# Optimization experiments

Hardware: AMD Instinct MI355X
Metric: run time of the kernel (lower is better)

Reference implementation:

```python
import jax, jax.numpy as jnp
import numpy as np

RADIUS = 0.4
NSHELLS = 3
GSCALE = 0.69314718056 * NSHELLS ** 2  # ln(2)*num_shells^2, as in TFN.__init__
KNN = 32          # patch_size
UNITS = 64        # per-type intertwiner width
STRIDE = 4        # source->target pooling ratio (num_points[i]/num_points[i+1])


def real_sh(d):
    """Real spherical harmonics up to l=3 on unit vectors d[...,3] -> [...,16]."""
    x, y, z = d[..., 0], d[..., 1], d[..., 2]
    x2, y2, z2 = x * x, y * y, z * z
    comps = [
        0.282095 * jnp.ones_like(x),                 # l=0
        0.488603 * y, 0.488603 * z, 0.488603 * x,    # l=1 (y,z,x)
        1.092548 * x * y,                            # l=2
        1.092548 * y * z,
        0.315392 * (3.0 * z2 - 1.0),
        1.092548 * x * z,
        0.546274 * (x2 - y2),
        0.590044 * y * (3.0 * x2 - y2),              # l=3
        2.890611 * x * y * z,
        0.457046 * y * (5.0 * z2 - 1.0),
        0.373176 * z * (5.0 * z2 - 3.0),
        0.457046 * x * (5.0 * z2 - 1.0),
        1.445306 * z * (x2 - y2),
        0.590044 * x * (x2 - 3.0 * y2),
    ]
    return jnp.stack(comps, axis=-1)


def setup_inputs() -> dict:
    key = jax.random.key(0)
    ks = jax.random.split(key, 16)
    B, N, C = 32, 2048, 64
    SC = NSHELLS * C  # channels after shell expansion
    FEAT = 4 * UNITS  # invariant feature dim (types 0..3)
    NUM_CLASSES = 40
    inp = {
        "points": jax.random.normal(ks[0], (B, N, 3), jnp.float32),
        "feats": 0.1 * jax.random.normal(ks[1], (B, N, C), jnp.float32),
        "W0": jax.random.normal(ks[2], (SC, UNITS), jnp.float32) / np.sqrt(SC),
        "b0": jnp.zeros((UNITS,), jnp.float32),
        "W1": jax.random.normal(ks[3], (SC, UNITS), jnp.float32) / np.sqrt(SC),
        "W2": jax.random.normal(ks[4], (SC, UNITS), jnp.float32) / np.sqrt(SC),
        "W3": jax.random.normal(ks[5], (SC, UNITS), jnp.float32) / np.sqrt(SC),
        "Wfc1": jax.random.normal(ks[6], (FEAT, 512), jnp.float32) / np.sqrt(FEAT),
        "bfc1": jnp.zeros((512,), jnp.float32),
        "Wfc2": jax.random.normal(ks[7], (512, 256), jnp.float32) / np.sqrt(512),
        "bfc2": jnp.zeros((256,), jnp.float32),
        "Wsm": jax.random.normal(ks[8], (256, NUM_CLASSES), jnp.float32) / np.sqrt(256),
        "bsm": jnp.zeros((NUM_CLASSES,), jnp.float32),
    }
    return inp


def reference(points, feats, W0, b0, W1, W2, W3, Wfc1, bfc1, Wfc2, bfc2, Wsm, bsm):
    # --- pooling: strided subsample (kd_pooling analogue) ---
    target = points[:, ::STRIDE]                       # [B,M,3]
    # --- ball-query style grouping: knn gather ---
    d2 = jnp.sum((target[:, :, None, :] - points[:, None, :, :]) ** 2, axis=-1)  # [B,M,N]
    _, idx = jax.lax.top_k(-d2, KNN)                   # [B,M,K]
    gat = jax.vmap(lambda a, i: a[i])
    p = gat(points, idx)                               # [B,M,K,3]
    f = gat(feats, idx)                                # [B,M,K,C]
    rel = p - target[:, :, None, :]
    dist = jnp.sqrt(jnp.maximum(jnp.sum(rel * rel, axis=-1), 1e-12))  # [B,M,K]
    dirs = rel / dist[..., None]
    # --- spherical-harmonic Gaussian shell kernels ---
    Y = real_sh(dirs)                                  # [B,M,K,16]
    centers = jnp.linspace(0.0, 1.0, NSHELLS)
    dn = dist / RADIUS
    w = jnp.exp(-GSCALE * (dn[..., None] - centers) ** 2)
    w = w * (dn <= 1.0)[..., None]                     # bounded kernel
    w = w / (jnp.sum(w, axis=2, keepdims=True) + 1e-8)  # normalize over patch
    kern = w[..., :, None] * Y[..., None, :]           # [B,M,K,S,16]
    # --- point conv: contract over patch dim ---
    z = jnp.einsum('bmksp,bmkc->bmpsc', kern, f)       # [B,M,16,S,C]
    B_, M_ = z.shape[:2]
    z = z.reshape(B_, M_, 16, -1)                      # [B,M,16,S*C]
    # --- per-type Dense intertwiners (bias only on type-0) + invariant norms ---
    slabs = [(0, 1, W0, b0), (1, 4, W1, None), (4, 9, W2, None), (9, 16, W3, None)]
    outs = []
    for s, e, W, b in slabs:
        o = z[:, :, s:e, :] @ W
        if b is not None:
            o = o + b
        outs.append(jnp.sqrt(jnp.maximum(jnp.sum(o * o, axis=2), 1e-8)))  # [B,M,U]
    h = jnp.concatenate(outs, axis=-1)                 # [B,M,4U]
    h = jnp.max(h, axis=1)                             # global max pool
    # --- MLP head ---
    h = jax.nn.relu(h @ Wfc1 + bfc1)
    h = jax.nn.relu(h @ Wfc2 + bfc2)
    return jax.nn.softmax(h @ Wsm + bsm, axis=-1)
```

## Files before the change

kernel.cpp:

```cpp
#include <hip/hip_runtime.h>
#include <hip/hip_bf16.h>
#include <math.h>

#define B_ 32
#define N_ 2048
#define C_ 64
#define M_ 512
#define KNN_ 32
#define RADIUS_ 0.4f
#define RCUT2 0.16016f
#define GSCALE_ 6.2383246250f
#define TT 4
#define NWAVE 8
#define SEGCAP 40
#define NBLK 4096

typedef __attribute__((ext_vector_type(8))) short bf16x8;
typedef __attribute__((ext_vector_type(4))) float f32x4;
union FragU { uint4 q; bf16x8 h; unsigned int u[4]; };

#define ZT_ 3144
#define RST 196
#define FSH 560
#define FSL 1616
#define CAND_OFF 6288
#define WGT_OFF  12576
#define WGT_TS   96
#define SM_TOTAL 12960

__device__ inline void split2(float a, unsigned& hi, unsigned& lo) {
    unsigned ab = __float_as_uint(a);
    float res = a - __uint_as_float(ab & 0xffff0000u);
    __hip_bfloat16 lb = __float2bfloat16(res);
    hi = ab >> 16;
    lo = *(unsigned short*)&lb;
}

__device__ inline unsigned cvt_pk_bf16(float a, float b) {
    unsigned r;
    asm("v_cvt_pk_bf16_f32 %0, %1, %2" : "=v"(r) : "v"(a), "v"(b));
    return r;
}

__device__ inline void split_pair(float a0, float a1, unsigned& hw, unsigned& lw) {
    hw = cvt_pk_bf16(a0, a1);
    float r0 = a0 - __uint_as_float(hw << 16);
    float r1 = a1 - __uint_as_float(hw & 0xffff0000u);
    lw = cvt_pk_bf16(r0, r1);
}

__device__ inline unsigned pack_hl(float a) {
    unsigned t = cvt_pk_bf16(a, a);
    unsigned hfu = t << 16;
    float res = a - __uint_as_float(hfu);
    return cvt_pk_bf16(__uint_as_float(hfu), res);
}

__global__ __launch_bounds__(256) void wsplit_kernel(
    const float* __restrict__ W0, const float* __restrict__ W1,
    const float* __restrict__ W2, const float* __restrict__ W3,
    uint4* __restrict__ Wb)
{
    int gid = blockIdx.x * 256 + threadIdx.x;
    int lane = gid & 63, frag = gid >> 6;
    int v = frag & 1, nt = (frag >> 1) & 3;
    int ls = frag >> 3, ks = ls % 6, l = ls / 6;
    const float* W = (l==0) ? W0 : (l==1) ? W1 : (l==2) ? W2 : W3;
    int n = nt*16 + (lane & 15), quad = lane >> 4;
    unsigned int d[4];
    #pragma unroll
    for (int dd = 0; dd < 4; ++dd) {
        unsigned int two[2];
        #pragma unroll
        for (int e = 0; e < 2; ++e) {
            int k = ks*32 + quad*8 + dd*2 + e;
            unsigned hi, lo;
            split2(W[k*64 + n], hi, lo);
            two[e] = (v == 0) ? hi : lo;
        }
        d[dd] = two[0] | (two[1] << 16);
    }
    Wb[(size_t)frag*64 + lane] = make_uint4(d[0], d[1], d[2], d[3]);
}

__global__ __launch_bounds__(512, 6) void main_kernel(
    const float* __restrict__ points, const float* __restrict__ feats,
    const float* __restrict__ b0, const uint4* __restrict__ Wb,
    unsigned int* __restrict__ hmax,
    const float* __restrict__ Wfc1, const float* __restrict__ Wfc2,
    float* __restrict__ dummy)
{
    __shared__ __align__(16) float smem[SM_TOTAL];
    __shared__ int sh_nbr[TT][32];
    __shared__ int sh_cnt[TT];
    __shared__ int cntk[NWAVE*TT];
    unsigned int* smemU = (unsigned int*)smem;
    const int tid = threadIdx.x;
    const int b = blockIdx.x >> 7;
    const int mbase = (blockIdx.x & 127) * TT;
    const float* pb = points + (size_t)b * N_ * 3;
    const int wv = tid >> 6, lane = tid & 63;

    float wm1 = Wfc1[(size_t)blockIdx.x*32 + (tid & 31)];
    float wm2 = Wfc2[(size_t)blockIdx.x*32 + (tid & 31)];

    const int nh_pre = wv >> 2;
    float b0r[2];
    #pragma unroll
    for (int ntl = 0; ntl < 2; ++ntl)
        b0r[ntl] = b0[(nh_pre*2 + ntl)*16 + (lane & 15)];

    {
        unsigned long long* cand = (unsigned long long*)&smem[CAND_OFF];
        float tx[TT], ty[TT], tz[TT];
        #pragma unroll
        for (int c = 0; c < TT; ++c) {
            int m4 = 4*(mbase + c);
            tx[c] = pb[3*m4]; ty[c] = pb[3*m4+1]; tz[c] = pb[3*m4+2];
        }
        float px[4], py[4], pz[4];
        const float* ps = pb + 3*(wv*256 + lane);
        #pragma unroll
        for (int it = 0; it < 4; ++it) {
            px[it] = ps[it*192+0]; py[it] = ps[it*192+1]; pz[it] = ps[it*192+2];
        }
        int bcnt[TT];
        #pragma unroll
        for (int c = 0; c < TT; ++c) bcnt[c] = 0;
        #pragma unroll
        for (int it = 0; it < 4; ++it) {
            int i = wv*256 + it*64 + lane;
            #pragma unroll
            for (int c = 0; c < TT; ++c) {
                float dx = px[it] - tx[c], dy = py[it] - ty[c], dz = pz[it] - tz[c];
                float d2 = fmaf(dx,dx, fmaf(dy,dy, dz*dz));
                bool isc = d2 <= RCUT2;
                unsigned long long mk = __ballot(isc);
                if (isc) {
                    int pos = bcnt[c] + __popcll(mk & ((1ull<<lane)-1ull));
                    if (pos < SEGCAP)
                        cand[(size_t)(wv*TT+c)*SEGCAP + pos] =
                            ((unsigned long long)__float_as_uint(d2) << 32) | (unsigned)i;
                }
                bcnt[c] += __popcll(mk);
            }
        }
        if (lane == 0) {
            #pragma unroll
            for (int c = 0; c < TT; ++c)
                cntk[wv*TT+c] = bcnt[c] < SEGCAP ? bcnt[c] : SEGCAP;
        }
    }
    __syncthreads();

    if (wv < TT) {
        unsigned long long* cand = (unsigned long long*)&smem[CAND_OFF];
        const int t = wv;
        int os[NWAVE+1];
        os[0] = 0;
        #pragma unroll
        for (int w = 0; w < NWAVE; ++w) os[w+1] = os[w] + cntk[w*TT+t];
        int C = os[NWAVE] < 128 ? os[NWAVE] : 128;
        auto fetch = [&](int pos) -> unsigned long long {
            if (pos >= C) return ~0ull;
            int ws = 0, base = 0;
            #pragma unroll
            for (int w = 1; w < NWAVE; ++w)
                if (pos >= os[w]) { ws = w; base = os[w]; }
            return cand[(size_t)(ws*TT+t)*SEGCAP + (pos - base)];
        };
        unsigned long long kv0 = fetch(lane), kv1 = fetch(64 + lane);
        const unsigned long long lmask = (1ull << lane) - 1ull;
        if (C <= KNN_) {
            if (lane < KNN_) sh_nbr[t][lane] = (lane < C) ? (int)(kv0 & 0xffffffffu) : 0;
            if (lane == 0) sh_cnt[t] = C;
        } else {
            unsigned d0 = (unsigned)(kv0 >> 32);
            unsigned d1 = (unsigned)(kv1 >> 32);
            unsigned thr = 0u;
            for (int bit = 29; bit >= 0; --bit) {
                unsigned mid = thr | (1u << bit);
                int cnt = __popcll(__ballot(d0 < mid)) + __popcll(__ballot(d1 < mid));
                if (cnt < KNN_) thr = mid;
            }
            bool le0 = d0 < thr, le1 = d1 < thr;
            int cntL = __popcll(__ballot(le0)) + __popcll(__ballot(le1));
            int E = KNN_ - cntL;
            unsigned long long me0 = __ballot(d0 == thr);
            unsigned long long me1 = __ballot(d1 == thr);
            int e0 = __popcll(me0);
            bool sel0 = le0 || ((d0 == thr) && (__popcll(me0 & lmask) < E));
            bool sel1 = le1 || ((d1 == thr) && (e0 + __popcll(me1 & lmask) < E));
            unsigned long long ms0 = __ballot(sel0);
            if (sel0) sh_nbr[t][__popcll(ms0 & lmask)] = (int)(kv0 & 0xffffffffu);
            int base0 = __popcll(ms0);
            unsigned long long ms1 = __ballot(sel1);
            if (sel1) sh_nbr[t][base0 + __popcll(ms1 & lmask)] = (int)(kv1 & 0xffffffffu);
            if (lane == 0) sh_cnt[t] = KNN_;
        }
    }
    __syncthreads();

    {
        const int t = wv & 3, kh = wv >> 2;
        const float* fb = feats + (size_t)b * N_ * C_;
        float fv0[8], fv1[8];
        #pragma unroll
        for (int j = 0; j < 8; ++j) {
            int k2 = kh*8 + j;
            fv0[j] = fb[(size_t)sh_nbr[t][2*k2]   * C_ + lane];
            fv1[j] = fb[(size_t)sh_nbr[t][2*k2+1] * C_ + lane];
        }
        if (wv < TT && lane < 32) {
            int k = lane;
            int n = sh_nbr[t][k];
            int m4 = 4*(mbase + t);
            float x = pb[3*n]   - pb[3*m4];
            float y = pb[3*n+1] - pb[3*m4+1];
            float z = pb[3*n+2] - pb[3*m4+2];
            float d2 = x*x + y*y + z*z;
            float dist = sqrtf(fmaxf(d2, 1e-12f));
            float inv = 1.0f / dist;
            float dx = x*inv, dy = y*inv, dz = z*inv;
            float x2 = dx*dx, y2 = dy*dy, z2 = dz*dz;
            float yv[16];
            yv[0]  = 0.282095f;
            yv[1]  = 0.488603f*dy;  yv[2] = 0.488603f*dz;  yv[3] = 0.488603f*dx;
            yv[4]  = 1.092548f*dx*dy;
            yv[5]  = 1.092548f*dy*dz;
            yv[6]  = 0.315392f*(3.0f*z2-1.0f);
            yv[7]  = 1.092548f*dx*dz;
            yv[8]  = 0.546274f*(x2-y2);
            yv[9]  = 0.590044f*dy*(3.0f*x2-y2);
            yv[10] = 2.890611f*dx*dy*dz;
            yv[11] = 0.457046f*dy*(5.0f*z2-1.0f);
            yv[12] = 0.373176f*dz*(5.0f*z2-3.0f);
            yv[13] = 0.457046f*dx*(5.0f*z2-1.0f);
            yv[14] = 1.445306f*dz*(x2-y2);
            yv[15] = 0.590044f*dx*(x2-3.0f*y2);
            float* Yp = &smem[t*ZT_ + k*17];
            #pragma unroll
            for (int p = 0; p < 16; ++p) Yp[p] = yv[p];
            float dn = dist * (1.0f/RADIUS_);
            bool ok = (k < sh_cnt[t]) && (dn <= 1.0f);
            float w0 = 0.f, w1 = 0.f, w2 = 0.f;
            if (ok) {
                float dd0 = dn, dd1 = dn - 0.5f, dd2 = dn - 1.0f;
                w0 = __expf(-GSCALE_*dd0*dd0);
                w1 = __expf(-GSCALE_*dd1*dd1);
                w2 = __expf(-GSCALE_*dd2*dd2);
            }
            float s0 = w0, s1 = w1, s2 = w2;
            #pragma unroll
            for (int off = 16; off >= 1; off >>= 1) {
                s0 += __shfl_xor(s0, off);
                s1 += __shfl_xor(s1, off);
                s2 += __shfl_xor(s2, off);
            }
            w0 /= (s0 + 1e-8f);
            w1 /= (s1 + 1e-8f);
            w2 /= (s2 + 1e-8f);
            smem[WGT_OFF + t*WGT_TS +      k] = w0;
            smem[WGT_OFF + t*WGT_TS + 32 + k] = w1;
            smem[WGT_OFF + t*WGT_TS + 64 + k] = w2;
        }
        #pragma unroll
        for (int j = 0; j < 8; ++j) {
            int k2 = kh*8 + j;
            unsigned hw, lw;
            split_pair(fv0[j], fv1[j], hw, lw);
            smemU[t*ZT_ + FSH + k2*66 + lane] = hw;
            smemU[t*ZT_ + FSL + k2*66 + lane] = lw;
        }
    }
    __syncthreads();

    f32x4 zacc[3][2];
    {
        const int t = wv & 3, nh = wv >> 2;
        const int quad = lane >> 4, col = lane & 15;
        float yv8[8];
        #pragma unroll
        for (int d = 0; d < 8; ++d)
            yv8[d] = smem[t*ZT_ + (quad*8 + d)*17 + col];
        FragU ah[3], al[3];
        #pragma unroll
        for (int s = 0; s < 3; ++s) {
            #pragma unroll
            for (int i = 0; i < 4; ++i) {
                float we = smem[WGT_OFF + t*WGT_TS + s*32 + quad*8 + 2*i];
                float wo = smem[WGT_OFF + t*WGT_TS + s*32 + quad*8 + 2*i + 1];
                split_pair(yv8[2*i]*we, yv8[2*i+1]*wo, ah[s].u[i], al[s].u[i]);
            }
        }
        #pragma unroll
        for (int s = 0; s < 3; ++s)
            #pragma unroll
            for (int nl = 0; nl < 2; ++nl) zacc[s][nl] = (f32x4){0.f,0.f,0.f,0.f};
        #pragma unroll
        for (int nl = 0; nl < 2; ++nl) {
            int n = (nh*2 + nl)*16 + col;
            FragU bh, bl;
            #pragma unroll
            for (int i = 0; i < 4; ++i) {
                int k2 = quad*4 + i;
                bh.u[i] = smemU[t*ZT_ + FSH + k2*66 + n];
                bl.u[i] = smemU[t*ZT_ + FSL + k2*66 + n];
            }
            #pragma unroll
            for (int s = 0; s < 3; ++s) {
                zacc[s][nl] = __builtin_amdgcn_mfma_f32_16x16x32_bf16(ah[s].h, bh.h, zacc[s][nl], 0, 0, 0);
                zacc[s][nl] = __builtin_amdgcn_mfma_f32_16x16x32_bf16(ah[s].h, bl.h, zacc[s][nl], 0, 0, 0);
                zacc[s][nl] = __builtin_amdgcn_mfma_f32_16x16x32_bf16(al[s].h, bh.h, zacc[s][nl], 0, 0, 0);
            }
        }
    }
    __syncthreads();

    {
        const int t = wv & 3, nh = wv >> 2;
        const int quad = lane >> 4, col = lane & 15;
        #pragma unroll
        for (int s = 0; s < 3; ++s) {
            #pragma unroll
            for (int nl = 0; nl < 2; ++nl) {
                #pragma unroll
                for (int r = 0; r < 4; ++r) {
                    int p = quad*4 + r;
                    smemU[t*ZT_ + p*RST + s*64 + (nh*2+nl)*16 + col] = pack_hl(zacc[s][nl][r]);
                }
            }
        }
    }
    __syncthreads();

    {
        const int bp0[4] = {0,1,4,9};
        const int bsz[4] = {1,3,5,7};
        const int band = wv & 3, nh = wv >> 2;
        const int sz = bsz[band], p0 = bp0[band];
        const int rows = 2*sz;
        const int quad = lane >> 4, col = lane & 15;
        int gc = col < rows-1 ? col : rows-1;
        int tl = gc >= sz ? 1 : 0;
        int pA = p0 + gc - tl*sz;
        const unsigned baseA = tl*ZT_ + pA*RST;
        const unsigned baseB = baseA + 2*ZT_;
        f32x4 acc[2][2];
        #pragma unroll
        for (int ti = 0; ti < 2; ++ti)
            #pragma unroll
            for (int ntl = 0; ntl < 2; ++ntl) acc[ti][ntl] = (f32x4){0.f,0.f,0.f,0.f};

        #pragma unroll
        for (int ks = 0; ks < 6; ++ks) {
            const uint4* zpA = (const uint4*)&smemU[baseA + ks*32 + quad*8];
            const uint4* zpB = (const uint4*)&smemU[baseB + ks*32 + quad*8];
            uint4 a0q = zpA[0], a1q = zpA[1];
            uint4 c0q = zpB[0], c1q = zpB[1];
            FragU ahA, alA, ahB, alB;
            ahA.u[0] = __builtin_amdgcn_perm(a0q.y, a0q.x, 0x05040100u);
            ahA.u[1] = __builtin_amdgcn_perm(a0q.w, a0q.z, 0x05040100u);
            ahA.u[2] = __builtin_amdgcn_perm(a1q.y, a1q.x, 0x05040100u);
            ahA.u[3] = __builtin_amdgcn_perm(a1q.w, a1q.z, 0x05040100u);
            alA.u[0] = __builtin_amdgcn_perm(a0q.y, a0q.x, 0x07060302u);
            alA.u[1] = __builtin_amdgcn_perm(a0q.w, a0q.z, 0x07060302u);
            alA.u[2] = __builtin_amdgcn_perm(a1q.y, a1q.x, 0x07060302u);
            alA.u[3] = __builtin_amdgcn_perm(a1q.w, a1q.z, 0x07060302u);
            ahB.u[0] = __builtin_amdgcn_perm(c0q.y, c0q.x, 0x05040100u);
            ahB.u[1] = __builtin_amdgcn_perm(c0q.w, c0q.z, 0x05040100u);
            ahB.u[2] = __builtin_amdgcn_perm(c1q.y, c1q.x, 0x05040100u);
            ahB.u[3] = __builtin_amdgcn_perm(c1q.w, c1q.z, 0x05040100u);
            alB.u[0] = __builtin_amdgcn_perm(c0q.y, c0q.x, 0x07060302u);
            alB.u[1] = __builtin_amdgcn_perm(c0q.w, c0q.z, 0x07060302u);
            alB.u[2] = __builtin_amdgcn_perm(c1q.y, c1q.x, 0x07060302u);
            alB.u[3] = __builtin_amdgcn_perm(c1q.w, c1q.z, 0x07060302u);
            #pragma unroll
            for (int ntl = 0; ntl < 2; ++ntl) {
                int fbase = ((band*6 + ks)*4 + nh*2 + ntl)*2;
                FragU bh, bl;
                bh.q = Wb[(size_t)(fbase + 0)*64 + lane];
                bl.q = Wb[(size_t)(fbase + 1)*64 + lane];
                acc[0][ntl] = __builtin_amdgcn_mfma_f32_16x16x32_bf16(ahA.h, bh.h, acc[0][ntl], 0, 0, 0);
                acc[0][ntl] = __builtin_amdgcn_mfma_f32_16x16x32_bf16(ahA.h, bl.h, acc[0][ntl], 0, 0, 0);
                acc[0][ntl] = __builtin_amdgcn_mfma_f32_16x16x32_bf16(alA.h, bh.h, acc[0][ntl], 0, 0, 0);
                acc[1][ntl] = __builtin_amdgcn_mfma_f32_16x16x32_bf16(ahB.h, bh.h, acc[1][ntl], 0, 0, 0);
                acc[1][ntl] = __builtin_amdgcn_mfma_f32_16x16x32_bf16(ahB.h, bl.h, acc[1][ntl], 0, 0, 0);
                acc[1][ntl] = __builtin_amdgcn_mfma_f32_16x16x32_bf16(alB.h, bh.h, acc[1][ntl], 0, 0, 0);
            }
        }
        float sq[2][4];
        #pragma unroll
        for (int ntl = 0; ntl < 2; ++ntl)
            #pragma unroll
            for (int tg = 0; tg < 4; ++tg) sq[ntl][tg] = 0.f;
        #pragma unroll
        for (int r = 0; r < 4; ++r) {
            int row = quad*4 + r;
            bool valid = row < rows;
            int tl2 = row >= sz ? 1 : 0;
            #pragma unroll
            for (int ti = 0; ti < 2; ++ti) {
                #pragma unroll
                for (int ntl = 0; ntl < 2; ++ntl) {
                    float o = acc[ti][ntl][r];
                    if (band == 0) o += b0r[ntl];
                    if (valid) sq[ntl][ti*2 + tl2] += o*o;
                }
            }
        }
        #pragma unroll
        for (int ntl = 0; ntl < 2; ++ntl) {
            #pragma unroll
            for (int tg = 0; tg < 4; ++tg) {
                float v = sq[ntl][tg];
                v += __shfl_xor(v, 16);
                v += __shfl_xor(v, 32);
                sq[ntl][tg] = v;
            }
        }
        if (quad == 0) {
            #pragma unroll
            for (int ntl = 0; ntl < 2; ++ntl) {
                float m = fmaxf(fmaxf(sq[ntl][0], sq[ntl][1]),
                                fmaxf(sq[ntl][2], sq[ntl][3]));
                float h = sqrtf(fmaxf(m, 1e-8f));
                atomicMax(&hmax[b*256 + band*64 + (nh*2 + ntl)*16 + col],
                          __float_as_uint(h) ^ 0x80000000u);
            }
        }
    }

    if (__float_as_uint(wm1 + wm2) == 0xdeadbeefu) dummy[0] = wm1;
}

__global__ __launch_bounds__(256) void fc1_kernel(
    const unsigned int* __restrict__ hmaxk,
    const float* __restrict__ Wfc1, const float* __restrict__ bfc1,
    float* __restrict__ t1)
{
    __shared__ float h[256];
    __shared__ float red[4][80];
    const int b = blockIdx.x >> 3, uc = blockIdx.x & 7;
    const int tid = threadIdx.x;
    const int u = tid & 63, iq = tid >> 6;
    h[tid] = __uint_as_float(hmaxk[b*256 + tid] ^ 0x80000000u);
    __syncthreads();
    float acc = 0.f;
    const float* Wp = Wfc1 + uc*64 + u;
    #pragma unroll 8
    for (int i = iq*64; i < iq*64 + 64; ++i)
        acc = fmaf(h[i], Wp[(size_t)i*512], acc);
    red[iq][u] = acc;
    __syncthreads();
    if (iq == 0) {
        float s = red[0][u] + red[1][u] + red[2][u] + red[3][u] + bfc1[uc*64 + u];
        t1[b*512 + uc*64 + u] = fmaxf(s, 0.f);
    }
}

__global__ __launch_bounds__(256) void fc2_kernel(
    const float* __restrict__ t1,
    const float* __restrict__ Wfc2, const float* __restrict__ bfc2,
    float* __restrict__ t2)
{
    __shared__ float t1s[512];
    __shared__ float red[4][80];
    const int b = blockIdx.x >> 2, uc = blockIdx.x & 3;
    const int tid = threadIdx.x;
    const int u = tid & 63, isl = tid >> 6;
    t1s[tid]       = t1[b*512 + tid];
    t1s[256 + tid] = t1[b*512 + 256 + tid];
    __syncthreads();
    float acc = 0.f;
    const float* Wp = Wfc2 + uc*64 + u;
    #pragma unroll 8
    for (int i = isl*128; i < isl*128 + 128; ++i)
        acc = fmaf(t1s[i], Wp[(size_t)i*256], acc);
    red[isl][u] = acc;
    __syncthreads();
    if (isl == 0) {
        float s = red[0][u] + red[1][u] + red[2][u] + red[3][u] + bfc2[uc*64 + u];
        t2[b*256 + uc*64 + u] = fmaxf(s, 0.f);
    }
}

__global__ __launch_bounds__(256) void fc3_kernel(
    const float* __restrict__ t2,
    const float* __restrict__ Wsm, const float* __restrict__ bsm,
    float* __restrict__ out)
{
    __shared__ float t2s[256];
    __shared__ float red[4][80];
    const int b = blockIdx.x;
    const int tid = threadIdx.x;
    const int u = tid & 63, isl = tid >> 6;
    t2s[tid] = t2[b*256 + tid];
    __syncthreads();
    float acc = 0.f;
    if (u < 40) {
        #pragma unroll 8
        for (int i = isl*64; i < isl*64 + 64; ++i)
            acc = fmaf(t2s[i], Wsm[(size_t)i*40 + u], acc);
    }
    red[isl][u] = acc;
    __syncthreads();
    if (tid < 64) {
        float s = red[0][tid] + red[1][tid] + red[2][tid] + red[3][tid];
        float x = (tid < 40) ? (s + bsm[tid]) : -1e30f;
        float mx = x;
        #pragma unroll
        for (int off = 32; off >= 1; off >>= 1) mx = fmaxf(mx, __shfl_xor(mx, off));
        float e = (tid < 40) ? expf(x - mx) : 0.f;
        float ssum = e;
        #pragma unroll
        for (int off = 32; off >= 1; off >>= 1) ssum += __shfl_xor(ssum, off);
        if (tid < 40) out[b*40 + tid] = e / ssum;
    }
}

extern "C" void kernel_launch(void* const* d_in, const int* in_sizes, int n_in,
                              void* d_out, int out_size, void* d_ws, size_t ws_size,
                              hipStream_t stream)
{
    const float* points = (const float*)d_in[0];
    const float* feats  = (const float*)d_in[1];
    const float* W0   = (const float*)d_in[2];
    const float* b0   = (const float*)d_in[3];
    const float* W1   = (const float*)d_in[4];
    const float* W2   = (const float*)d_in[5];
    const float* W3   = (const float*)d_in[6];
    const float* Wfc1 = (const float*)d_in[7];
    const float* bfc1 = (const float*)d_in[8];
    const float* Wfc2 = (const float*)d_in[9];
    const float* bfc2 = (const float*)d_in[10];
    const float* Wsm  = (const float*)d_in[11];
    const float* bsm  = (const float*)d_in[12];
    float* out = (float*)d_out;

    char* ws = (char*)d_ws;
    unsigned int* hmax = (unsigned int*)ws;
    float* t1 = (float*)(ws + 32*1024);
    float* t2 = (float*)(ws + 96*1024);
    float* dummy = (float*)(ws + 120*1024);
    uint4* Wb = (uint4*)(ws + 128*1024);

    wsplit_kernel<<<48, 256, 0, stream>>>(W0, W1, W2, W3, Wb);
    main_kernel<<<NBLK, 512, 0, stream>>>(points, feats, b0, Wb, hmax,
                                          Wfc1, Wfc2, dummy);
    fc1_kernel<<<256, 256, 0, stream>>>(hmax, Wfc1, bfc1, t1);
    fc2_kernel<<<128, 256, 0, stream>>>(t1, Wfc2, bfc2, t2);
    fc3_kernel<<<32, 256, 0, stream>>>(t2, Wsm, bsm, out);
}
```

Before: 178.7 us.

## Use single bf16 weights in intertwiner MFMA and prefetch weight fragments

Weight matrices are now converted to a single rounded bf16 copy instead of a hi/lo split, which cuts the intertwiner MFMA count from six to four per step and halves the weight-fragment loads. Weight fragments for the next k-step are prefetched into registers ahead of use, and the first fragment load is issued before the barrier so global-load latency overlaps the synchronisation. The cost is lower precision in the weight product (activations are still split hi/lo), which could affect accuracy, plus extra live registers.

```diff
diff --git a/kernel.cpp b/kernel.cpp
--- a/kernel.cpp
+++ b/kernel.cpp
@@ -28,14 +28,6 @@
 #define WGT_TS   96
 #define SM_TOTAL 12960
 
-__device__ inline void split2(float a, unsigned& hi, unsigned& lo) {
-    unsigned ab = __float_as_uint(a);
-    float res = a - __uint_as_float(ab & 0xffff0000u);
-    __hip_bfloat16 lb = __float2bfloat16(res);
-    hi = ab >> 16;
-    lo = *(unsigned short*)&lb;
-}
-
 __device__ inline unsigned cvt_pk_bf16(float a, float b) {
     unsigned r;
     asm("v_cvt_pk_bf16_f32 %0, %1, %2" : "=v"(r) : "v"(a), "v"(b));
@@ -63,8 +55,8 @@
 {
     int gid = blockIdx.x * 256 + threadIdx.x;
     int lane = gid & 63, frag = gid >> 6;
-    int v = frag & 1, nt = (frag >> 1) & 3;
-    int ls = frag >> 3, ks = ls % 6, l = ls / 6;
+    int nt = frag & 3;
+    int ls = frag >> 2, ks = ls % 6, l = ls / 6;
     const float* W = (l==0) ? W0 : (l==1) ? W1 : (l==2) ? W2 : W3;
     int n = nt*16 + (lane & 15), quad = lane >> 4;
     unsigned int d[4];
@@ -74,9 +66,8 @@
         #pragma unroll
         for (int e = 0; e < 2; ++e) {
             int k = ks*32 + quad*8 + dd*2 + e;
-            unsigned hi, lo;
-            split2(W[k*64 + n], hi, lo);
-            two[e] = (v == 0) ? hi : lo;
+            __hip_bfloat16 hb = __float2bfloat16(W[k*64 + n]);
+            two[e] = *(unsigned short*)&hb;
         }
         d[dd] = two[0] | (two[1] << 16);
     }
@@ -332,12 +323,17 @@
             }
         }
     }
-    __syncthreads();
 
     {
         const int bp0[4] = {0,1,4,9};
         const int bsz[4] = {1,3,5,7};
         const int band = wv & 3, nh = wv >> 2;
+        FragU bcur[2], bnxt[2];
+        #pragma unroll
+        for (int ntl = 0; ntl < 2; ++ntl)
+            bcur[ntl].q = Wb[(size_t)((band*6 + 0)*4 + nh*2 + ntl)*64 + lane];
+        __syncthreads();
+
         const int sz = bsz[band], p0 = bp0[band];
         const int rows = 2*sz;
         const int quad = lane >> 4, col = lane & 15;
@@ -354,6 +350,11 @@
 
         #pragma unroll
         for (int ks = 0; ks < 6; ++ks) {
+            if (ks < 5) {
+                #pragma unroll
+                for (int ntl = 0; ntl < 2; ++ntl)
+                    bnxt[ntl].q = Wb[(size_t)((band*6 + ks+1)*4 + nh*2 + ntl)*64 + lane];
+            }
             const uint4* zpA = (const uint4*)&smemU[baseA + ks*32 + quad*8];
             const uint4* zpB = (const uint4*)&smemU[baseB + ks*32 + quad*8];
             uint4 a0q = zpA[0], a1q = zpA[1];
@@ -377,17 +378,13 @@
             alB.u[3] = __builtin_amdgcn_perm(c1q.w, c1q.z, 0x07060302u);
             #pragma unroll
             for (int ntl = 0; ntl < 2; ++ntl) {
-                int fbase = ((band*6 + ks)*4 + nh*2 + ntl)*2;
-                FragU bh, bl;
-                bh.q = Wb[(size_t)(fbase + 0)*64 + lane];
-                bl.q = Wb[(size_t)(fbase + 1)*64 + lane];
-                acc[0][ntl] = __builtin_amdgcn_mfma_f32_16x16x32_bf16(ahA.h, bh.h, acc[0][ntl], 0, 0, 0);
-                acc[0][ntl] = __builtin_amdgcn_mfma_f32_16x16x32_bf16(ahA.h, bl.h, acc[0][ntl], 0, 0, 0);
-                acc[0][ntl] = __builtin_amdgcn_mfma_f32_16x16x32_bf16(alA.h, bh.h, acc[0][ntl], 0, 0, 0);
-                acc[1][ntl] = __builtin_amdgcn_mfma_f32_16x16x32_bf16(ahB.h, bh.h, acc[1][ntl], 0, 0, 0);
-                acc[1][ntl] = __builtin_amdgcn_mfma_f32_16x16x32_bf16(ahB.h, bl.h, acc[1][ntl], 0, 0, 0);
-                acc[1][ntl] = __builtin_amdgcn_mfma_f32_16x16x32_bf16(alB.h, bh.h, acc[1][ntl], 0, 0, 0);
-            }
+                acc[0][ntl] = __builtin_amdgcn_mfma_f32_16x16x32_bf16(ahA.h, bcur[ntl].h, acc[0][ntl], 0, 0, 0);
+                acc[0][ntl] = __builtin_amdgcn_mfma_f32_16x16x32_bf16(alA.h, bcur[ntl].h, acc[0][ntl], 0, 0, 0);
+                acc[1][ntl] = __builtin_amdgcn_mfma_f32_16x16x32_bf16(ahB.h, bcur[ntl].h, acc[1][ntl], 0, 0, 0);
+                acc[1][ntl] = __builtin_amdgcn_mfma_f32_16x16x32_bf16(alB.h, bcur[ntl].h, acc[1][ntl], 0, 0, 0);
+            }
+            #pragma unroll
+            for (int ntl = 0; ntl < 2; ++ntl) bcur[ntl] = bnxt[ntl];
         }
         float sq[2][4];
         #pragma unroll
@@ -545,7 +542,7 @@
     float* dummy = (float*)(ws + 120*1024);
     uint4* Wb = (uint4*)(ws + 128*1024);
 
-    wsplit_kernel<<<48, 256, 0, stream>>>(W0, W1, W2, W3, Wb);
+    wsplit_kernel<<<24, 256, 0, stream>>>(W0, W1, W2, W3, Wb);
     main_kernel<<<NBLK, 512, 0, stream>>>(points, feats, b0, Wb, hmax,
                                           Wfc1, Wfc2, dummy);
     fc1_kernel<<<256, 256, 0, stream>>>(hmax, Wfc1, bfc1, t1);
```

Result: faster. 168.2 us (-5.8%).
